# Kernel optimization log

Measured on AMD Instinct MI355X. Metric: run time of the kernel, lower is better.

The kernel has to match this reference:

```python
import jax, jax.numpy as jnp
import numpy as np

N_EMB = 1024
N_HEAD = 16
HEAD_DIM = N_EMB // N_HEAD


def setup_inputs() -> dict:
    key = jax.random.key(0)
    ks = jax.random.split(key, 5)
    scale = 0.02
    x = jax.random.normal(ks[0], (2, 2048, N_EMB), dtype=jnp.float32)
    W_attn = jax.random.normal(ks[1], (N_EMB, 3 * N_EMB), dtype=jnp.float32) * scale
    b_attn = jnp.zeros((3 * N_EMB,), dtype=jnp.float32)
    W_proj = jax.random.normal(ks[2], (N_EMB, N_EMB), dtype=jnp.float32) * scale
    b_proj = jnp.zeros((N_EMB,), dtype=jnp.float32)
    return {"x": x, "W_attn": W_attn, "b_attn": b_attn, "W_proj": W_proj, "b_proj": b_proj}


def reference(x, W_attn, b_attn, W_proj, b_proj):
    B, T, C = x.shape
    qkv = x @ W_attn + b_attn  # [B, T, 3C]
    q, k, v = jnp.split(qkv, 3, axis=-1)
    # [B, H, T, Dh]
    q = q.reshape(B, T, N_HEAD, HEAD_DIM).transpose(0, 2, 1, 3)
    k = k.reshape(B, T, N_HEAD, HEAD_DIM).transpose(0, 2, 1, 3)
    v = v.reshape(B, T, N_HEAD, HEAD_DIM).transpose(0, 2, 1, 3)
    scale = 1.0 / jnp.sqrt(jnp.float32(HEAD_DIM))
    attn = jnp.einsum('bhqd,bhkd->bhqk', q, k) * scale  # [B, H, T, T]
    causal = jnp.tril(jnp.ones((T, T), dtype=bool))
    attn = jnp.where(causal[None, None], attn, -jnp.inf)
    attn = jax.nn.softmax(attn, axis=-1)
    y = jnp.einsum('bhqk,bhkd->bhqd', attn, v)  # [B, H, T, Dh]
    y = y.transpose(0, 2, 1, 3).reshape(B, T, C)
    return y @ W_proj + b_proj
```

## Files before the change

kernel.cpp:

```cpp
#include <hip/hip_runtime.h>
#include <hip/hip_bf16.h>

typedef __bf16 bf16;
typedef __attribute__((ext_vector_type(2))) __bf16 bf16x2;
typedef __attribute__((ext_vector_type(4))) __bf16 bf16x4;
typedef __attribute__((ext_vector_type(8))) __bf16 bf16x8;
typedef __attribute__((ext_vector_type(4))) float f32x4;
typedef __attribute__((ext_vector_type(16))) float f32x16;
typedef unsigned int u32;
typedef __attribute__((ext_vector_type(4))) u32 u32x4;
typedef const __attribute__((address_space(1))) u32* gptr_t;
typedef __attribute__((address_space(3))) u32* lptr_t;

#define N_EMB 1024
#define N_HEAD 16
#define HEAD_DIM 64
#define T_SEQ 2048
#define BATCH 2
#define M_TOT (BATCH * T_SEQ)
#define N_QKV (3 * N_EMB)
#define KDIM 1024
#define CS_LOG2E 0.1803368801111129f

__device__ inline unsigned short f2bu(float f) {
    unsigned u = __builtin_bit_cast(unsigned, f);
    return (unsigned short)((u + 0x7fffu + ((u >> 16) & 1u)) >> 16);
}
__device__ inline bf16 f2b(float f) {
    unsigned short s = f2bu(f);
    return __builtin_bit_cast(bf16, s);
}
__device__ inline u32 pkbf(float lo, float hi) {
    bf16x2 t; t[0] = (bf16)lo; t[1] = (bf16)hi;
    return __builtin_bit_cast(u32, t);
}
__device__ __forceinline__ float xhalf_sum(float x) {
    return x + __shfl_xor(x, 32, 64);
}

__global__ __launch_bounds__(256) void k_cast(const float* __restrict__ x,
                                              bf16* __restrict__ xb, int n4) {
    int i = blockIdx.x * 256 + threadIdx.x;
    if (i < n4) {
        float4 v = reinterpret_cast<const float4*>(x)[i];
        ushort4 u;
        u.x = f2bu(v.x); u.y = f2bu(v.y); u.z = f2bu(v.z); u.w = f2bu(v.w);
        reinterpret_cast<ushort4*>(xb)[i] = u;
    }
}

__global__ __launch_bounds__(256) void k_transpose(const float* __restrict__ W,
                                                   bf16* __restrict__ Wt,
                                                   int K, int N) {
    __shared__ float tile[32][33];
    int k0 = blockIdx.x * 32;
    int n0 = blockIdx.y * 32;
    int tx = threadIdx.x & 31;
    int ty = threadIdx.x >> 5;
    for (int j = 0; j < 32; j += 8)
        tile[ty + j][tx] = W[(k0 + ty + j) * N + n0 + tx];
    __syncthreads();
    for (int j = 0; j < 32; j += 8)
        Wt[(n0 + ty + j) * (long)K + k0 + tx] = f2b(tile[tx][ty + j]);
}

__global__ __launch_bounds__(256) void k_vtrans(const bf16* __restrict__ v,
                                                bf16* __restrict__ vt) {
    __shared__ bf16 tile[64 * 76];
    const int bh = blockIdx.y;
    const int t0 = blockIdx.x * 64;
    const bf16* src = v + (size_t)bh * T_SEQ * HEAD_DIM;
    bf16* dst = vt + (size_t)bh * HEAD_DIM * T_SEQ;
    const int tid = threadIdx.x;
    #pragma unroll
    for (int it = 0; it < 2; ++it) {
        const int row = (tid >> 3) + it * 32;
        const int col = (tid & 7) * 8;
        bf16x8 val = *reinterpret_cast<const bf16x8*>(src + (size_t)(t0 + row) * HEAD_DIM + col);
        bf16x4 lo;  lo[0] = val[0]; lo[1] = val[1]; lo[2] = val[2]; lo[3] = val[3];
        bf16x4 hiv; hiv[0] = val[4]; hiv[1] = val[5]; hiv[2] = val[6]; hiv[3] = val[7];
        *reinterpret_cast<bf16x4*>(&tile[row * 76 + col]) = lo;
        *reinterpret_cast<bf16x4*>(&tile[row * 76 + col + 4]) = hiv;
    }
    __syncthreads();
    #pragma unroll
    for (int it = 0; it < 2; ++it) {
        const int d  = (tid >> 3) + it * 32;
        const int tt = (tid & 7) * 8;
        bf16x8 val;
        #pragma unroll
        for (int q = 0; q < 8; ++q) {
            const int pq = tt + q;
            const int sw = ((pq >> 2) ^ (pq >> 3)) & 1;
            const int ps = sw ? (pq ^ 12) : pq;
            val[q] = tile[ps * 76 + d];
        }
        *reinterpret_cast<bf16x8*>(dst + (size_t)d * T_SEQ + t0 + tt) = val;
    }
}

#define GEMM_MAINLOOP(A_, Bt_, m0_, n0_)                                          \
    __shared__ __align__(16) bf16 As[128 * 32];                                   \
    __shared__ __align__(16) bf16 Bs[128 * 32];                                   \
    const int lane = threadIdx.x & 63;                                            \
    const int w    = threadIdx.x >> 6;                                            \
    const int wr   = w >> 1;                                                      \
    const int wc   = w & 1;                                                       \
    const int r    = lane & 15;                                                   \
    const int ko   = (lane >> 4) * 8;                                             \
    const int srow = w * 32 + (lane >> 2);                                        \
    const int sk   = (lane & 3) * 8;                                              \
    const bf16* a_g0 = A_ + (size_t)(m0_ + srow) * KDIM + sk;                     \
    const bf16* a_g1 = a_g0 + 16 * KDIM;                                          \
    const bf16* b_g0 = Bt_ + (size_t)(n0_ + srow) * KDIM + sk;                    \
    const bf16* b_g1 = b_g0 + 16 * KDIM;                                          \
    bf16* a_l0 = As + (w * 2) * 512;                                              \
    bf16* a_l1 = As + (w * 2 + 1) * 512;                                          \
    bf16* b_l0 = Bs + (w * 2) * 512;                                              \
    bf16* b_l1 = Bs + (w * 2 + 1) * 512;                                          \
    f32x4 acc[4][4];                                                              \
    for (int i = 0; i < 4; ++i)                                                   \
        for (int j = 0; j < 4; ++j) acc[i][j] = (f32x4){0.f, 0.f, 0.f, 0.f};      \
    for (int k0 = 0; k0 < KDIM; k0 += 32) {                                       \
        __builtin_amdgcn_global_load_lds((gptr_t)(const void*)(a_g0 + k0),        \
                                         (lptr_t)(void*)a_l0, 16, 0, 0);          \
        __builtin_amdgcn_global_load_lds((gptr_t)(const void*)(a_g1 + k0),        \
                                         (lptr_t)(void*)a_l1, 16, 0, 0);          \
        __builtin_amdgcn_global_load_lds((gptr_t)(const void*)(b_g0 + k0),        \
                                         (lptr_t)(void*)b_l0, 16, 0, 0);          \
        __builtin_amdgcn_global_load_lds((gptr_t)(const void*)(b_g1 + k0),        \
                                         (lptr_t)(void*)b_l1, 16, 0, 0);          \
        __syncthreads();                                                          \
        bf16x8 af[4], bfr[4];                                                     \
        for (int m = 0; m < 4; ++m)                                               \
            af[m] = *reinterpret_cast<const bf16x8*>(As + (wr * 64 + m * 16 + r) * 32 + ko); \
        for (int n = 0; n < 4; ++n)                                               \
            bfr[n] = *reinterpret_cast<const bf16x8*>(Bs + (wc * 64 + n * 16 + r) * 32 + ko); \
        for (int m = 0; m < 4; ++m)                                               \
            for (int n = 0; n < 4; ++n)                                           \
                acc[m][n] = __builtin_amdgcn_mfma_f32_16x16x32_bf16(af[m], bfr[n], acc[m][n], 0, 0, 0); \
        __syncthreads();                                                          \
    }

#define GEMM_MAINLOOP_64(A_, Bt_, m0_, n0_)                                       \
    __shared__ __align__(16) bf16 As[64 * 32];                                    \
    __shared__ __align__(16) bf16 Bs[128 * 32];                                   \
    const int lane = threadIdx.x & 63;                                            \
    const int w    = threadIdx.x >> 6;                                            \
    const int wr   = w >> 1;                                                      \
    const int wc   = w & 1;                                                       \
    const int r    = lane & 15;                                                   \
    const int ko   = (lane >> 4) * 8;                                             \
    const int srow = w * 16 + (lane >> 2);                                        \
    const int sk   = (lane & 3) * 8;                                              \
    const bf16* a_g0 = A_ + (size_t)(m0_ + srow) * KDIM + sk;                     \
    const bf16* b_g0 = Bt_ + (size_t)(n0_ + srow) * KDIM + sk;                    \
    const bf16* b_g1 = b_g0 + 64 * KDIM;                                          \
    bf16* a_l0 = As + w * 512;                                                    \
    bf16* b_l0 = Bs + w * 512;                                                    \
    bf16* b_l1 = Bs + 64 * 32 + w * 512;                                          \
    f32x4 acc[2][4];                                                              \
    for (int i = 0; i < 2; ++i)                                                   \
        for (int j = 0; j < 4; ++j) acc[i][j] = (f32x4){0.f, 0.f, 0.f, 0.f};      \
    for (int k0 = 0; k0 < KDIM; k0 += 32) {                                       \
        __builtin_amdgcn_global_load_lds((gptr_t)(const void*)(a_g0 + k0),        \
                                         (lptr_t)(void*)a_l0, 16, 0, 0);          \
        __builtin_amdgcn_global_load_lds((gptr_t)(const void*)(b_g0 + k0),        \
                                         (lptr_t)(void*)b_l0, 16, 0, 0);          \
        __builtin_amdgcn_global_load_lds((gptr_t)(const void*)(b_g1 + k0),        \
                                         (lptr_t)(void*)b_l1, 16, 0, 0);          \
        __syncthreads();                                                          \
        bf16x8 af[2], bfr[4];                                                     \
        for (int m = 0; m < 2; ++m)                                               \
            af[m] = *reinterpret_cast<const bf16x8*>(As + (wr * 32 + m * 16 + r) * 32 + ko); \
        for (int n = 0; n < 4; ++n)                                               \
            bfr[n] = *reinterpret_cast<const bf16x8*>(Bs + (wc * 64 + n * 16 + r) * 32 + ko); \
        for (int m = 0; m < 2; ++m)                                               \
            for (int n = 0; n < 4; ++n)                                           \
                acc[m][n] = __builtin_amdgcn_mfma_f32_16x16x32_bf16(af[m], bfr[n], acc[m][n], 0, 0, 0); \
        __syncthreads();                                                          \
    }

__global__ __launch_bounds__(256) void k_gemm_qkv(const bf16* __restrict__ A,
                                                  const bf16* __restrict__ Bt,
                                                  const float* __restrict__ bias,
                                                  bf16* __restrict__ qb,
                                                  bf16* __restrict__ kb,
                                                  bf16* __restrict__ vb) {
    const int m0 = blockIdx.x * 128;
    const int n0 = blockIdx.y * 128;
    GEMM_MAINLOOP(A, Bt, m0, n0)
    const int col   = lane & 15;
    const int rbase = (lane >> 4) * 4;
    for (int nn = 0; nn < 4; ++nn) {
        int n = n0 + wc * 64 + nn * 16 + col;
        float bv = bias[n];
        int which = n >> 10;
        int c  = n & 1023;
        int h  = c >> 6;
        int dh = c & 63;
        bf16* dst = (which == 0) ? qb : ((which == 1) ? kb : vb);
        const float sc = (which == 0) ? CS_LOG2E : 1.0f;
        for (int mm = 0; mm < 4; ++mm) {
            for (int i = 0; i < 4; ++i) {
                int m = m0 + wr * 64 + mm * 16 + rbase + i;
                int b_ = m >> 11;
                int t  = m & 2047;
                dst[(((b_ * N_HEAD + h) * T_SEQ) + t) * HEAD_DIM + dh] =
                    f2b((acc[mm][nn][i] + bv) * sc);
            }
        }
    }
}

__global__ __launch_bounds__(256) void k_gemm_proj(const bf16* __restrict__ A,
                                                   const bf16* __restrict__ Bt,
                                                   const float* __restrict__ bias,
                                                   float* __restrict__ out) {
    const int m0 = blockIdx.x * 64;
    const int n0 = blockIdx.y * 128;
    GEMM_MAINLOOP_64(A, Bt, m0, n0)
    const int col   = lane & 15;
    const int rbase = (lane >> 4) * 4;
    for (int nn = 0; nn < 4; ++nn) {
        int n = n0 + wc * 64 + nn * 16 + col;
        float bv = bias[n];
        for (int mm = 0; mm < 2; ++mm) {
            for (int i = 0; i < 4; ++i) {
                int m = m0 + wr * 32 + mm * 16 + rbase + i;
                out[(size_t)m * N_EMB + n] = acc[mm][nn][i] + bv;
            }
        }
    }
}

__device__ __forceinline__ void pv_group(const float* p,
                                         const bf16x8 (&va)[2][2], f32x16 (&o)[2]) {
    u32x4 f0, f1;
    f0[0] = pkbf(p[0], p[1]);   f0[1] = pkbf(p[2], p[3]);
    f0[2] = pkbf(p[4], p[5]);   f0[3] = pkbf(p[6], p[7]);
    f1[0] = pkbf(p[8], p[9]);   f1[1] = pkbf(p[10], p[11]);
    f1[2] = pkbf(p[12], p[13]); f1[3] = pkbf(p[14], p[15]);
    bf16x8 pb0 = __builtin_bit_cast(bf16x8, f0);
    bf16x8 pb1 = __builtin_bit_cast(bf16x8, f1);
    __builtin_amdgcn_s_setprio(1);
    #pragma unroll
    for (int dt = 0; dt < 2; ++dt) {
        o[dt] = __builtin_amdgcn_mfma_f32_32x32x16_bf16(va[dt][0], pb0, o[dt], 0, 0, 0);
        o[dt] = __builtin_amdgcn_mfma_f32_32x32x16_bf16(va[dt][1], pb1, o[dt], 0, 0, 0);
    }
    __builtin_amdgcn_s_setprio(0);
}

__device__ __forceinline__ void stage_k32(const char* Kg, char* Ks, int kbase, int lane) {
    #pragma unroll
    for (int rr = 0; rr < 4; ++rr) {
        const int fb  = rr * 1024 + lane * 16;
        const int row = fb >> 7;
        const int swz = (row & 7) << 4;
        __builtin_amdgcn_global_load_lds(
            (gptr_t)(const void*)(Kg + (size_t)kbase * 128 + (fb ^ swz)),
            (lptr_t)(void*)(Ks + rr * 1024), 16, 0, 0);
    }
}
__device__ __forceinline__ void stage_v32(const char* Vg, char* Vs, int kbase, int lane) {
    #pragma unroll
    for (int rr = 0; rr < 4; ++rr) {
        const int fb  = rr * 1024 + lane * 16;
        const int d   = fb >> 6;
        const int off = fb & 63;
        const int swz = (d & 3) << 4;
        __builtin_amdgcn_global_load_lds(
            (gptr_t)(const void*)(Vg + (size_t)d * (T_SEQ * 2) + (size_t)kbase * 2 + (off ^ swz)),
            (lptr_t)(void*)(Vs + rr * 1024), 16, 0, 0);
    }
}

__device__ __forceinline__ void tile32_w(const char* Ks, const char* Vs,
                                         int qr, int hi, const bf16x8 (&qf)[4],
                                         bool diag, float& l_r, f32x16 (&o)[2]) {
    const int swzk = (qr & 7) << 4;
    bf16x8 kf[4];
    #pragma unroll
    for (int f = 0; f < 4; ++f)
        kf[f] = *reinterpret_cast<const bf16x8*>(
            Ks + ((qr * 128 + f * 32 + hi * 16) ^ swzk));
    f32x16 st;
    #pragma unroll
    for (int r = 0; r < 16; ++r) st[r] = 0.f;
    __builtin_amdgcn_s_setprio(1);
    #pragma unroll
    for (int f = 0; f < 4; ++f)
        st = __builtin_amdgcn_mfma_f32_32x32x16_bf16(kf[f], qf[f], st, 0, 0, 0);
    __builtin_amdgcn_s_setprio(0);
    if (diag) {
        const int kp4 = 4 * hi;
        #pragma unroll
        for (int r = 0; r < 16; ++r) {
            const int kpos = (r & 3) + 8 * (r >> 2) + kp4;
            if (kpos > qr) st[r] = -3.0e38f;
        }
    }
    bf16x8 va[2][2];
    #pragma unroll
    for (int dt = 0; dt < 2; ++dt)
        #pragma unroll
        for (int ks = 0; ks < 2; ++ks) {
            const int d = dt * 32 + qr;
            va[dt][ks] = *reinterpret_cast<const bf16x8*>(
                Vs + ((d * 64 + ks * 32 + hi * 16) ^ ((d & 3) << 4)));
        }
    float p[16];
    #pragma unroll
    for (int r = 0; r < 16; ++r) p[r] = exp2f(fminf(st[r], 24.f));
    float s = 0.f;
    #pragma unroll
    for (int r = 0; r < 8; ++r) s += p[r] + p[r + 8];
    l_r += s;
    pv_group(p, va, o);
}

__global__ __launch_bounds__(256) void k_attn(const bf16* __restrict__ qb,
                                              const bf16* __restrict__ kb,
                                              const bf16* __restrict__ vtb,
                                              bf16* __restrict__ yb) {
    const int lane = threadIdx.x & 63;
    const int wv   = threadIdx.x >> 6;
    const int bh   = blockIdx.x;
    const int qblk = 63 - blockIdx.y;
    const int q0   = qblk * 32;
    const int b    = bh >> 4;
    const int h    = bh & 15;

    const char* Qg = (const char*)(qb  + (size_t)bh * T_SEQ * HEAD_DIM);
    const char* Kg = (const char*)(kb  + (size_t)bh * T_SEQ * HEAD_DIM);
    const char* Vg = (const char*)(vtb + (size_t)bh * HEAD_DIM * T_SEQ);

    const int qr = lane & 31;
    const int hi = lane >> 5;

    __shared__ __align__(16) char sbuf[4][8192];
    __shared__ float ls_l[4][64];
    char* Ks = sbuf[wv];
    char* Vs = sbuf[wv] + 4096;

    stage_k32(Qg, Ks, qblk * 32, lane);
    asm volatile("s_waitcnt vmcnt(0)" ::: "memory");
    bf16x8 qf[4];
    {
        const int swzk = (qr & 7) << 4;
        #pragma unroll
        for (int f = 0; f < 4; ++f)
            qf[f] = *reinterpret_cast<const bf16x8*>(
                Ks + ((qr * 128 + f * 32 + hi * 16) ^ swzk));
    }

    f32x16 o[2];
    #pragma unroll
    for (int r = 0; r < 16; ++r) { o[0][r] = 0.f; o[1][r] = 0.f; }
    float l_r = 0.f;

    const int n    = qblk + 1;
    const int base = n >> 2;
    const int rem  = n & 3;
    const int lo   = wv * base + (wv < rem ? wv : rem);
    const int cnt  = base + (wv < rem ? 1 : 0);
    const int end  = lo + cnt;

    for (int t = lo; t < end; ++t) {
        stage_k32(Kg, Ks, t * 32, lane);
        stage_v32(Vg, Vs, t * 32, lane);
        asm volatile("s_waitcnt vmcnt(0)" ::: "memory");
        tile32_w(Ks, Vs, qr, hi, qf, t == qblk, l_r, o);
    }

    float* slab = (float*)sbuf[wv];
    if (wv > 0) {
        #pragma unroll
        for (int i = 0; i < 16; ++i) {
            slab[i * 64 + lane]        = o[0][i];
            slab[(16 + i) * 64 + lane] = o[1][i];
        }
        ls_l[wv][lane] = l_r;
    }
    __syncthreads();
    if (wv > 0) return;
    #pragma unroll
    for (int s = 1; s < 4; ++s) {
        const float* sl = (const float*)sbuf[s];
        l_r += ls_l[s][lane];
        #pragma unroll
        for (int i = 0; i < 16; ++i) {
            o[0][i] += sl[i * 64 + lane];
            o[1][i] += sl[(16 + i) * 64 + lane];
        }
    }
    l_r = xhalf_sum(l_r);

    const float inv = 1.f / fmaxf(l_r, 1e-30f);
    const int tq = q0 + qr;
    bf16* yrow = yb + ((size_t)(b * T_SEQ + tq)) * N_EMB + h * HEAD_DIM;
    #pragma unroll
    for (int dt = 0; dt < 2; ++dt) {
        #pragma unroll
        for (int rr = 0; rr < 4; ++rr) {
            const int d0 = dt * 32 + 8 * rr + 4 * hi;
            ushort4 u;
            u.x = f2bu(o[dt][4 * rr + 0] * inv);
            u.y = f2bu(o[dt][4 * rr + 1] * inv);
            u.z = f2bu(o[dt][4 * rr + 2] * inv);
            u.w = f2bu(o[dt][4 * rr + 3] * inv);
            *reinterpret_cast<ushort4*>(yrow + d0) = u;
        }
    }
}

extern "C" void kernel_launch(void* const* d_in, const int* in_sizes, int n_in,
                              void* d_out, int out_size, void* d_ws, size_t ws_size,
                              hipStream_t stream) {
    const float* x      = (const float*)d_in[0];
    const float* W_attn = (const float*)d_in[1];
    const float* b_attn = (const float*)d_in[2];
    const float* W_proj = (const float*)d_in[3];
    const float* b_proj = (const float*)d_in[4];
    float* out = (float*)d_out;

    const size_t sz_x   = (size_t)M_TOT * N_EMB;
    const size_t sz_wat = (size_t)N_QKV * N_EMB;
    const size_t sz_wpt = (size_t)N_EMB * N_EMB;
    const size_t sz_hd  = (size_t)BATCH * N_HEAD * T_SEQ * HEAD_DIM;
    const size_t need = (sz_x + sz_wat + sz_wpt + 3 * sz_hd + sz_x) * sizeof(bf16);
    if (ws_size < need) return;

    bf16* xb  = (bf16*)d_ws;
    bf16* wat = xb + sz_x;
    bf16* wpt = wat + sz_wat;
    bf16* qb  = wpt + sz_wpt;
    bf16* kbf = qb + sz_hd;
    bf16* vbf = kbf + sz_hd;
    bf16* yb  = vbf + sz_hd;
    bf16* vtb = xb;

    k_cast<<<dim3((sz_x / 4 + 255) / 256), 256, 0, stream>>>(x, xb, (int)(sz_x / 4));
    k_transpose<<<dim3(N_EMB / 32, N_QKV / 32), 256, 0, stream>>>(W_attn, wat, N_EMB, N_QKV);
    k_transpose<<<dim3(N_EMB / 32, N_EMB / 32), 256, 0, stream>>>(W_proj, wpt, N_EMB, N_EMB);
    k_gemm_qkv<<<dim3(M_TOT / 128, N_QKV / 128), 256, 0, stream>>>(xb, wat, b_attn, qb, kbf, vbf);
    k_vtrans<<<dim3(T_SEQ / 64, BATCH * N_HEAD), 256, 0, stream>>>(vbf, vtb);
    k_attn<<<dim3(BATCH * N_HEAD, 64), 256, 0, stream>>>(qb, kbf, vtb, yb);
    k_gemm_proj<<<dim3(M_TOT / 64, N_EMB / 128), 256, 0, stream>>>(yb, wpt, b_proj, out);
}
```

Before: 117.3 us.

## Prefetch next K/V tile into registers while computing current attention tile

Replaces the synchronous global-to-LDS staging loop with a software pipeline. The next K and V tile is loaded into registers before the current tile's MFMA and softmax work, then written to LDS after compute, with an LDS wait fence in between. This is meant to hide global memory latency behind compute, at the cost of extra VGPRs and plain register stores in place of direct LDS loads. It also drops the fminf clamp before exp2f and shrinks the partial-sum scratch array.

```diff
diff --git a/kernel.cpp b/kernel.cpp
--- a/kernel.cpp
+++ b/kernel.cpp
@@ -36,6 +36,10 @@
 }
 __device__ __forceinline__ float xhalf_sum(float x) {
     return x + __shfl_xor(x, 32, 64);
+}
+__device__ __forceinline__ void lds_fence() {
+    asm volatile("s_waitcnt lgkmcnt(0)" ::: "memory");
+    __builtin_amdgcn_sched_barrier(0);
 }
 
 __global__ __launch_bounds__(256) void k_cast(const float* __restrict__ x,
@@ -276,6 +280,38 @@
     }
 }
 
+__device__ __forceinline__ void prefetch_k32(const char* Kg, int kbase, int lane,
+                                             bf16x8 (&kr)[4]) {
+    #pragma unroll
+    for (int rr = 0; rr < 4; ++rr) {
+        const int fb  = rr * 1024 + lane * 16;
+        const int row = fb >> 7;
+        const int swz = (row & 7) << 4;
+        kr[rr] = *reinterpret_cast<const bf16x8*>(
+            Kg + (size_t)kbase * 128 + (fb ^ swz));
+    }
+}
+__device__ __forceinline__ void prefetch_v32(const char* Vg, int kbase, int lane,
+                                             bf16x8 (&vr)[4]) {
+    #pragma unroll
+    for (int rr = 0; rr < 4; ++rr) {
+        const int fb  = rr * 1024 + lane * 16;
+        const int d   = fb >> 6;
+        const int off = fb & 63;
+        const int swz = (d & 3) << 4;
+        vr[rr] = *reinterpret_cast<const bf16x8*>(
+            Vg + (size_t)d * (T_SEQ * 2) + (size_t)kbase * 2 + (off ^ swz));
+    }
+}
+__device__ __forceinline__ void write_kv(char* Ks, char* Vs, int lane,
+                                         const bf16x8 (&kr)[4], const bf16x8 (&vr)[4]) {
+    #pragma unroll
+    for (int rr = 0; rr < 4; ++rr) {
+        *reinterpret_cast<bf16x8*>(Ks + rr * 1024 + lane * 16) = kr[rr];
+        *reinterpret_cast<bf16x8*>(Vs + rr * 1024 + lane * 16) = vr[rr];
+    }
+}
+
 __device__ __forceinline__ void tile32_w(const char* Ks, const char* Vs,
                                          int qr, int hi, const bf16x8 (&qf)[4],
                                          bool diag, float& l_r, f32x16 (&o)[2]) {
@@ -312,7 +348,7 @@
         }
     float p[16];
     #pragma unroll
-    for (int r = 0; r < 16; ++r) p[r] = exp2f(fminf(st[r], 24.f));
+    for (int r = 0; r < 16; ++r) p[r] = exp2f(st[r]);
     float s = 0.f;
     #pragma unroll
     for (int r = 0; r < 8; ++r) s += p[r] + p[r + 8];
@@ -340,7 +376,7 @@
     const int hi = lane >> 5;
 
     __shared__ __align__(16) char sbuf[4][8192];
-    __shared__ float ls_l[4][64];
+    __shared__ float ls_l[3][64];
     char* Ks = sbuf[wv];
     char* Vs = sbuf[wv] + 4096;
 
@@ -354,6 +390,7 @@
             qf[f] = *reinterpret_cast<const bf16x8*>(
                 Ks + ((qr * 128 + f * 32 + hi * 16) ^ swzk));
     }
+    lds_fence();
 
     f32x16 o[2];
     #pragma unroll
@@ -367,11 +404,23 @@
     const int cnt  = base + (wv < rem ? 1 : 0);
     const int end  = lo + cnt;
 
-    for (int t = lo; t < end; ++t) {
-        stage_k32(Kg, Ks, t * 32, lane);
-        stage_v32(Vg, Vs, t * 32, lane);
+    if (cnt > 0) {
+        stage_k32(Kg, Ks, lo * 32, lane);
+        stage_v32(Vg, Vs, lo * 32, lane);
         asm volatile("s_waitcnt vmcnt(0)" ::: "memory");
-        tile32_w(Ks, Vs, qr, hi, qf, t == qblk, l_r, o);
+        for (int t = lo; t < end; ++t) {
+            bf16x8 kr[4], vr[4];
+            const bool pf = (t + 1 < end);
+            if (pf) {
+                prefetch_k32(Kg, (t + 1) * 32, lane, kr);
+                prefetch_v32(Vg, (t + 1) * 32, lane, vr);
+            }
+            tile32_w(Ks, Vs, qr, hi, qf, t == qblk, l_r, o);
+            if (pf) {
+                write_kv(Ks, Vs, lane, kr, vr);
+                lds_fence();
+            }
+        }
     }
 
     float* slab = (float*)sbuf[wv];
@@ -381,14 +430,14 @@
             slab[i * 64 + lane]        = o[0][i];
             slab[(16 + i) * 64 + lane] = o[1][i];
         }
-        ls_l[wv][lane] = l_r;
+        ls_l[wv - 1][lane] = l_r;
     }
     __syncthreads();
     if (wv > 0) return;
     #pragma unroll
     for (int s = 1; s < 4; ++s) {
         const float* sl = (const float*)sbuf[s];
-        l_r += ls_l[s][lane];
+        l_r += ls_l[s - 1][lane];
         #pragma unroll
         for (int i = 0; i < 16; ++i) {
             o[0][i] += sl[i * 64 + lane];
```

Measured after the change: 126.3 us. +7.7%, slower.
